# Kernel tuning notes

Hardware: AMD Instinct MI355X
Metric: run time of the kernel (lower is better)

## Reference

```python
import jax, jax.numpy as jnp
import numpy as np

B, S, D, H = 4, 2048, 1024, 16
HD = D // H  # head_dim = 64

def setup_inputs() -> dict:
    key = jax.random.key(0)
    ks = jax.random.split(key, 5)
    scale = 1.0 / np.sqrt(D)
    return {
        "x": jax.random.normal(ks[0], (B, S, D), dtype=jnp.float32),
        "Wqkv": jax.random.normal(ks[1], (D, 3 * D), dtype=jnp.float32) * scale,
        "bqkv": jax.random.normal(ks[2], (3 * D,), dtype=jnp.float32) * 0.01,
        "Wo": jax.random.normal(ks[3], (D, D), dtype=jnp.float32) * scale,
        "bo": jax.random.normal(ks[4], (D,), dtype=jnp.float32) * 0.01,
    }

def reference(x, Wqkv, bqkv, Wo, bo):
    b, s, d = x.shape
    # fused QKV projection: [B,S,3D]
    qkv = jnp.einsum("bsd,de->bse", x, Wqkv) + bqkv
    # [B,S,H,3*HD] -> [B,H,S,3*HD], then chunk into q,k,v per head
    qkv = qkv.reshape(b, s, H, 3 * HD).transpose(0, 2, 1, 3)
    q, k, v = jnp.split(qkv, 3, axis=-1)  # each [B,H,S,HD]
    inv_sqrt_dk = jnp.asarray(1.0 / np.sqrt(HD), dtype=x.dtype)
    scores = jnp.einsum("bhqd,bhkd->bhqk", q, k) * inv_sqrt_dk
    attn = jax.nn.softmax(scores, axis=-1)
    values = jnp.einsum("bhqk,bhkd->bhqd", attn, v)  # [B,H,S,HD]
    # NOTE: source reshapes [B,H,S,HD] -> [B,S,H*HD] WITHOUT permuting back
    # (a quirk of the original code); replicated faithfully.
    values = values.reshape(b, s, d)
    out = jnp.einsum("bsd,de->bse", values, Wo) + bo
    return out
```

## Files before the change

### kernel.cpp

```cpp
#include <hip/hip_runtime.h>
#include <hip/hip_bf16.h>
#include <cstdint>

static constexpr int Bq  = 4;
static constexpr int Sq  = 2048;
static constexpr int Dq  = 1024;
static constexpr int Hq  = 16;
static constexpr int HDq = 64;
static constexpr int ROWS = Bq * Sq;
static constexpr int QKV_N = 3 * Dq;

typedef __bf16 bf16x8 __attribute__((ext_vector_type(8)));
typedef __bf16 bf16x4 __attribute__((ext_vector_type(4)));
typedef float  floatx4 __attribute__((ext_vector_type(4)));

#define MFMA16(a, b, c) __builtin_amdgcn_mfma_f32_16x16x32_bf16((a), (b), (c), 0, 0, 0)

#define QSCALE 0.18033688011112042f

__device__ __forceinline__ void async16(const void* g, void* l) {
    __builtin_amdgcn_global_load_lds(
        (const __attribute__((address_space(1))) uint32_t*)g,
        (__attribute__((address_space(3))) uint32_t*)l, 16, 0, 0);
}

__global__ __launch_bounds__(256) void cvt4_kernel(const float4* __restrict__ in,
                                                   bf16x4* __restrict__ out, int n4) {
    int i = blockIdx.x * 256 + threadIdx.x;
    if (i < n4) {
        float4 v = in[i];
        bf16x4 o;
        o[0] = (__bf16)v.x; o[1] = (__bf16)v.y; o[2] = (__bf16)v.z; o[3] = (__bf16)v.w;
        out[i] = o;
    }
}

__global__ __launch_bounds__(256) void tcvt_kernel(const float* __restrict__ in,
                                                   __bf16* __restrict__ out, int K, int N) {
    __shared__ float t[32][33];
    int n0 = blockIdx.x * 32, k0 = blockIdx.y * 32;
    int c = threadIdx.x & 31, r0 = threadIdx.x >> 5;
#pragma unroll
    for (int rr = 0; rr < 32; rr += 8)
        t[r0 + rr][c] = in[(size_t)(k0 + r0 + rr) * N + n0 + c];
    __syncthreads();
#pragma unroll
    for (int rr = 0; rr < 32; rr += 8)
        out[(size_t)(n0 + r0 + rr) * K + k0 + c] = (__bf16)t[c][r0 + rr];
}

template <int MODE>
__global__ __launch_bounds__(256) void gemm_bt_kernel(const __bf16* __restrict__ A,
                                                      const __bf16* __restrict__ BT,
                                                      const float* __restrict__ bias,
                                                      void* __restrict__ Cout,
                                                      __bf16* __restrict__ Vt,
                                                      int M, int N, int K) {
    __shared__ __bf16 As[128 * 32];
    __shared__ __bf16 Bs[128 * 32];

    const int t = threadIdx.x;
    const int lane = t & 63;
    const int wave = t >> 6;
    const int wm = wave & 1, wn = wave >> 1;
    const int l15 = lane & 15;
    const int kg = (lane >> 4) * 8;

    const int m0 = blockIdx.y * 128;
    const int n0 = blockIdx.x * 128;

    const int srow = t >> 2;
    const int scol = (t & 3) * 8;
    const __bf16* ag = A  + (size_t)(m0 + srow) * K + scol;
    const __bf16* bg = BT + (size_t)(n0 + srow) * K + scol;
    __bf16* al = As + t * 8;
    __bf16* bl = Bs + t * 8;

    floatx4 acc[4][4] = {};

    for (int k0 = 0; k0 < K; k0 += 32) {
        __syncthreads();
        async16(ag + k0,                    al);
        async16(ag + (size_t)64 * K + k0,   al + 2048);
        async16(bg + k0,                    bl);
        async16(bg + (size_t)64 * K + k0,   bl + 2048);
        __syncthreads();

        bf16x8 af[4], bfr[4];
#pragma unroll
        for (int mi = 0; mi < 4; ++mi)
            af[mi] = *(const bf16x8*)(As + (wm * 64 + mi * 16 + l15) * 32 + kg);
#pragma unroll
        for (int ni = 0; ni < 4; ++ni)
            bfr[ni] = *(const bf16x8*)(Bs + (wn * 64 + ni * 16 + l15) * 32 + kg);
#pragma unroll
        for (int mi = 0; mi < 4; ++mi)
#pragma unroll
            for (int ni = 0; ni < 4; ++ni)
                acc[mi][ni] = MFMA16(af[mi], bfr[ni], acc[mi][ni]);
    }

    const int r0 = (lane >> 4) * 4;
    const int wn0 = n0 + wn * 64;

    if (MODE == 2 && (wn0 % 192) == 128) {
#pragma unroll
        for (int ni = 0; ni < 4; ++ni) {
            int col = wn0 + ni * 16 + l15;
            float bv = bias[col];
            int h = col / 192;
            int d = col - h * 192 - 128;
#pragma unroll
            for (int mi = 0; mi < 4; ++mi) {
                int row = m0 + wm * 64 + mi * 16 + r0;
                int b = row >> 11, s = row & 2047;
                bf16x4 vv;
#pragma unroll
                for (int i = 0; i < 4; ++i) vv[i] = (__bf16)(acc[mi][ni][i] + bv);
                *(bf16x4*)(Vt + ((size_t)(b * Hq + h) * HDq + d) * Sq + s) = vv;
            }
        }
    } else {
        const float sc = (MODE == 2 && (wn0 % 192) == 0) ? QSCALE : 1.0f;
#pragma unroll
        for (int ni = 0; ni < 4; ++ni) {
            int col = wn0 + ni * 16 + l15;
            float bv = bias[col];
#pragma unroll
            for (int mi = 0; mi < 4; ++mi) {
#pragma unroll
                for (int i = 0; i < 4; ++i) {
                    int row = m0 + wm * 64 + mi * 16 + r0 + i;
                    float v = (acc[mi][ni][i] + bv) * sc;
                    size_t off = (size_t)row * N + col;
                    if (MODE == 1) ((float*)Cout)[off] = v;
                    else           ((__bf16*)Cout)[off] = (__bf16)v;
                }
            }
        }
    }
}

__global__ __launch_bounds__(256, 4) void attn_kernel(const __bf16* __restrict__ qkv,
                                                      const __bf16* __restrict__ Vt,
                                                      __bf16* __restrict__ v2) {
    const int bh = blockIdx.y;
    const int b = bh >> 4, h = bh & 15;
    const int q0 = blockIdx.x * 128;
    const int tid = threadIdx.x;
    const int lane = tid & 63;
    const int wave = tid >> 6;
    const int l15 = lane & 15;
    const int quad = lane >> 4;
    const int kg = quad * 8;
    const size_t rs = QKV_N;
    const __bf16* base  = qkv + (size_t)b * Sq * rs + (size_t)h * (3 * HDq);
    const __bf16* vbase = Vt + (size_t)bh * HDq * Sq;

    __shared__ alignas(16) __bf16 Ks[64][72];
    __shared__ alignas(16) __bf16 Vs[64][72];
    __shared__ alignas(16) __bf16 PT[8][16][72];

    bf16x8 qa[2][2];
#pragma unroll
    for (int qt = 0; qt < 2; ++qt) {
        const __bf16* qr = base + (size_t)(q0 + qt * 64 + wave * 16 + l15) * rs;
        qa[qt][0] = *(const bf16x8*)(qr + kg);
        qa[qt][1] = *(const bf16x8*)(qr + 32 + kg);
    }

    const int sd = tid >> 2;
    const int sc = (tid & 3) * 8;
    const __bf16* kgp = base + 64 + sc;
    const __bf16* vgp = vbase + (size_t)sd * Sq + sc;

    bf16x8 kr0 = *(const bf16x8*)(kgp + (size_t)sd * rs);
    bf16x8 kr1 = *(const bf16x8*)(kgp + (size_t)sd * rs + 32);
    bf16x8 vr0 = *(const bf16x8*)(vgp);
    bf16x8 vr1 = *(const bf16x8*)(vgp + 32);

    floatx4 o[2][4] = {};
    float l_acc[2] = {0.f, 0.f};

    for (int kt = 0; kt < Sq; kt += 64) {
        __syncthreads();
        *(bf16x8*)(&Ks[sd][sc])      = kr0;
        *(bf16x8*)(&Ks[sd][sc + 32]) = kr1;
        *(bf16x8*)(&Vs[sd][sc])      = vr0;
        *(bf16x8*)(&Vs[sd][sc + 32]) = vr1;
        __syncthreads();

        const int ktn = (kt + 64) & (Sq - 1);
        kr0 = *(const bf16x8*)(kgp + (size_t)(ktn + sd) * rs);
        kr1 = *(const bf16x8*)(kgp + (size_t)(ktn + sd) * rs + 32);
        vr0 = *(const bf16x8*)(vgp + ktn);
        vr1 = *(const bf16x8*)(vgp + ktn + 32);

        floatx4 s[2][4];
#pragma unroll
        for (int tt = 0; tt < 4; ++tt) {
            bf16x8 k0 = *(const bf16x8*)(&Ks[tt * 16 + l15][kg]);
            bf16x8 k1 = *(const bf16x8*)(&Ks[tt * 16 + l15][32 + kg]);
#pragma unroll
            for (int qt = 0; qt < 2; ++qt) {
                floatx4 z = {};
                z = MFMA16(k0, qa[qt][0], z);
                s[qt][tt] = MFMA16(k1, qa[qt][1], z);
            }
        }

#pragma unroll
        for (int qt = 0; qt < 2; ++qt) {
            float lsum = 0.f;
#pragma unroll
            for (int tt = 0; tt < 4; ++tt) {
                bf16x4 pp;
#pragma unroll
                for (int i = 0; i < 4; ++i) {
                    float p = __builtin_amdgcn_exp2f(s[qt][tt][i]);
                    lsum += p;
                    pp[i] = (__bf16)p;
                }
                *(bf16x4*)(&PT[qt * 4 + wave][l15][tt * 16 + quad * 4]) = pp;
            }
            l_acc[qt] += lsum;
        }

#pragma unroll
        for (int ks = 0; ks < 2; ++ks) {
            bf16x8 vb[4];
#pragma unroll
            for (int tt = 0; tt < 4; ++tt)
                vb[tt] = *(const bf16x8*)(&Vs[tt * 16 + l15][ks * 32 + kg]);
#pragma unroll
            for (int qt = 0; qt < 2; ++qt) {
                bf16x8 pa = *(const bf16x8*)(&PT[qt * 4 + wave][l15][ks * 32 + kg]);
#pragma unroll
                for (int tt = 0; tt < 4; ++tt)
                    o[qt][tt] = MFMA16(vb[tt], pa, o[qt][tt]);
            }
        }
    }

    float rinv[2];
#pragma unroll
    for (int qt = 0; qt < 2; ++qt) {
        float l = l_acc[qt];
        l += __shfl_xor(l, 16);
        l += __shfl_xor(l, 32);
        rinv[qt] = 1.0f / l;
    }

#pragma unroll
    for (int qt = 0; qt < 2; ++qt) {
        int q = q0 + qt * 64 + wave * 16 + l15;
        size_t row = (size_t)b * Sq + h * 128 + (q >> 4);
        __bf16* vrow = v2 + row * Dq + (size_t)(q & 15) * 64;
#pragma unroll
        for (int tt = 0; tt < 4; ++tt) {
            bf16x4 ov;
#pragma unroll
            for (int i = 0; i < 4; ++i)
                ov[i] = (__bf16)(o[qt][tt][i] * rinv[qt]);
            *(bf16x4*)(vrow + tt * 16 + quad * 4) = ov;
        }
    }
}

extern "C" void kernel_launch(void* const* d_in, const int* in_sizes, int n_in,
                              void* d_out, int out_size, void* d_ws, size_t ws_size,
                              hipStream_t stream) {
    const float* x    = (const float*)d_in[0];
    const float* Wqkv = (const float*)d_in[1];
    const float* bqkv = (const float*)d_in[2];
    const float* Wo   = (const float*)d_in[3];
    const float* bo   = (const float*)d_in[4];
    float* out = (float*)d_out;

    __bf16* xb    = (__bf16*)d_ws;
    __bf16* WqkvT = xb    + (size_t)ROWS * Dq;
    __bf16* WoT   = WqkvT + (size_t)QKV_N * Dq;
    __bf16* qkvb  = WoT   + (size_t)Dq * Dq;
    __bf16* Vt    = qkvb  + (size_t)ROWS * QKV_N;
    __bf16* v2    = xb;

    const int nx4 = ROWS * Dq / 4;
    cvt4_kernel<<<(nx4 + 255) / 256, 256, 0, stream>>>((const float4*)x, (bf16x4*)xb, nx4);
    tcvt_kernel<<<dim3(QKV_N / 32, Dq / 32), 256, 0, stream>>>(Wqkv, WqkvT, Dq, QKV_N);
    tcvt_kernel<<<dim3(Dq / 32, Dq / 32), 256, 0, stream>>>(Wo, WoT, Dq, Dq);

    gemm_bt_kernel<2><<<dim3(QKV_N / 128, ROWS / 128), 256, 0, stream>>>(
        xb, WqkvT, bqkv, (void*)qkvb, Vt, ROWS, QKV_N, Dq);

    attn_kernel<<<dim3(Sq / 128, Bq * Hq), 256, 0, stream>>>(qkvb, Vt, v2);

    gemm_bt_kernel<1><<<dim3(Dq / 128, ROWS / 128), 256, 0, stream>>>(
        v2, WoT, bo, (void*)out, nullptr, ROWS, Dq, Dq);
}
```

Before: 288.7 us.

## Load K/V fragments directly from global into registers, drop LDS staging and barriers

The attention kernel now has each wave load its K and V MFMA operand fragments straight from global memory into registers, instead of staging K/V tiles through shared memory with two block barriers per key tile. The Vt buffer row pitch is padded to 2112 elements, apparently to avoid cache or channel conflicts across head-dim rows. This removes LDS traffic and synchronisation, but each of the four waves now re-reads the same K/V data from L2/L1 with less coalesced, strided access. The software prefetch of the next tile is also gone, so load latency is exposed unless occupancy hides it. The Vt allocation must match the padded size, which the visible code does not show.

After: 450.8 us. 56.1% more time.

```diff
diff --git a/kernel.cpp b/kernel.cpp
--- a/kernel.cpp
+++ b/kernel.cpp
@@ -9,6 +9,7 @@
 static constexpr int HDq = 64;
 static constexpr int ROWS = Bq * Sq;
 static constexpr int QKV_N = 3 * Dq;
+static constexpr int VP   = 2112;
 
 typedef __bf16 bf16x8 __attribute__((ext_vector_type(8)));
 typedef __bf16 bf16x4 __attribute__((ext_vector_type(4)));
@@ -117,7 +118,7 @@
                 bf16x4 vv;
 #pragma unroll
                 for (int i = 0; i < 4; ++i) vv[i] = (__bf16)(acc[mi][ni][i] + bv);
-                *(bf16x4*)(Vt + ((size_t)(b * Hq + h) * HDq + d) * Sq + s) = vv;
+                *(bf16x4*)(Vt + ((size_t)(b * Hq + h) * HDq + d) * VP + s) = vv;
             }
         }
     } else {
@@ -147,19 +148,16 @@
     const int bh = blockIdx.y;
     const int b = bh >> 4, h = bh & 15;
     const int q0 = blockIdx.x * 128;
-    const int tid = threadIdx.x;
-    const int lane = tid & 63;
-    const int wave = tid >> 6;
+    const int lane = threadIdx.x & 63;
+    const int wave = threadIdx.x >> 6;
     const int l15 = lane & 15;
     const int quad = lane >> 4;
     const int kg = quad * 8;
     const size_t rs = QKV_N;
     const __bf16* base  = qkv + (size_t)b * Sq * rs + (size_t)h * (3 * HDq);
-    const __bf16* vbase = Vt + (size_t)bh * HDq * Sq;
-
-    __shared__ alignas(16) __bf16 Ks[64][72];
-    __shared__ alignas(16) __bf16 Vs[64][72];
-    __shared__ alignas(16) __bf16 PT[8][16][72];
+    const __bf16* vbase = Vt + (size_t)bh * HDq * VP;
+
+    __shared__ alignas(16) __bf16 PT[4][2][16][72];
 
     bf16x8 qa[2][2];
 #pragma unroll
@@ -169,43 +167,41 @@
         qa[qt][1] = *(const bf16x8*)(qr + 32 + kg);
     }
 
-    const int sd = tid >> 2;
-    const int sc = (tid & 3) * 8;
-    const __bf16* kgp = base + 64 + sc;
-    const __bf16* vgp = vbase + (size_t)sd * Sq + sc;
-
-    bf16x8 kr0 = *(const bf16x8*)(kgp + (size_t)sd * rs);
-    bf16x8 kr1 = *(const bf16x8*)(kgp + (size_t)sd * rs + 32);
-    bf16x8 vr0 = *(const bf16x8*)(vgp);
-    bf16x8 vr1 = *(const bf16x8*)(vgp + 32);
+    const __bf16* kp[4];
+    const __bf16* vp[4];
+#pragma unroll
+    for (int tt = 0; tt < 4; ++tt) {
+        kp[tt] = base + HDq + (size_t)(tt * 16 + l15) * rs + kg;
+        vp[tt] = vbase + (size_t)(tt * 16 + l15) * VP + kg;
+    }
 
     floatx4 o[2][4] = {};
     float l_acc[2] = {0.f, 0.f};
 
     for (int kt = 0; kt < Sq; kt += 64) {
-        __syncthreads();
-        *(bf16x8*)(&Ks[sd][sc])      = kr0;
-        *(bf16x8*)(&Ks[sd][sc + 32]) = kr1;
-        *(bf16x8*)(&Vs[sd][sc])      = vr0;
-        *(bf16x8*)(&Vs[sd][sc + 32]) = vr1;
-        __syncthreads();
-
-        const int ktn = (kt + 64) & (Sq - 1);
-        kr0 = *(const bf16x8*)(kgp + (size_t)(ktn + sd) * rs);
-        kr1 = *(const bf16x8*)(kgp + (size_t)(ktn + sd) * rs + 32);
-        vr0 = *(const bf16x8*)(vgp + ktn);
-        vr1 = *(const bf16x8*)(vgp + ktn + 32);
+        bf16x8 ka0[4], ka1[4];
+#pragma unroll
+        for (int tt = 0; tt < 4; ++tt) {
+            ka0[tt] = *(const bf16x8*)(kp[tt]);
+            ka1[tt] = *(const bf16x8*)(kp[tt] + 32);
+            kp[tt] += (size_t)64 * rs;
+        }
+        bf16x8 va0[4], va1[4];
+#pragma unroll
+        for (int tt = 0; tt < 4; ++tt) {
+            va0[tt] = *(const bf16x8*)(vp[tt]);
+            va1[tt] = *(const bf16x8*)(vp[tt] + 32);
+            vp[tt] += 64;
+        }
 
         floatx4 s[2][4];
 #pragma unroll
         for (int tt = 0; tt < 4; ++tt) {
-            bf16x8 k0 = *(const bf16x8*)(&Ks[tt * 16 + l15][kg]);
-            bf16x8 k1 = *(const bf16x8*)(&Ks[tt * 16 + l15][32 + kg]);
 #pragma unroll
             for (int qt = 0; qt < 2; ++qt) {
                 floatx4 z = {};
-                z = MFMA16(k0, qa[qt][0], z);
-                s[qt][tt] = MFMA16(k1, qa[qt][1], z);
+                z = MFMA16(ka0[tt], qa[qt][0], z);
+                s[qt][tt] = MFMA16(ka1[tt], qa[qt][1], z);
             }
         }
 
@@ -221,23 +217,19 @@
                     lsum += p;
                     pp[i] = (__bf16)p;
                 }
-                *(bf16x4*)(&PT[qt * 4 + wave][l15][tt * 16 + quad * 4]) = pp;
+                *(bf16x4*)(&PT[wave][qt][l15][tt * 16 + quad * 4]) = pp;
             }
             l_acc[qt] += lsum;
         }
 
 #pragma unroll
-        for (int ks = 0; ks < 2; ++ks) {
-            bf16x8 vb[4];
-#pragma unroll
-            for (int tt = 0; tt < 4; ++tt)
-                vb[tt] = *(const bf16x8*)(&Vs[tt * 16 + l15][ks * 32 + kg]);
-#pragma unroll
-            for (int qt = 0; qt < 2; ++qt) {
-                bf16x8 pa = *(const bf16x8*)(&PT[qt * 4 + wave][l15][ks * 32 + kg]);
-#pragma unroll
-                for (int tt = 0; tt < 4; ++tt)
-                    o[qt][tt] = MFMA16(vb[tt], pa, o[qt][tt]);
+        for (int qt = 0; qt < 2; ++qt) {
+            bf16x8 pa0 = *(const bf16x8*)(&PT[wave][qt][l15][kg]);
+            bf16x8 pa1 = *(const bf16x8*)(&PT[wave][qt][l15][32 + kg]);
+#pragma unroll
+            for (int tt = 0; tt < 4; ++tt) {
+                o[qt][tt] = MFMA16(va0[tt], pa0, o[qt][tt]);
+                o[qt][tt] = MFMA16(va1[tt], pa1, o[qt][tt]);
             }
         }
     }
```

## Enlarge attention query tile, double-buffer K/V in LDS, pad V transpose pitch

Applied to the files above, without the earlier changes.

Each attention block now handles 256 queries (4 query tiles per wave), so every K/V tile loaded into LDS is reused across twice as many queries. K/V shared buffers are double-buffered so only one barrier per iteration is needed. The transposed V buffer uses a padded row pitch to reduce memory channel conflicts. This trades higher register use, lower occupancy and fewer blocks per CU for more reuse and fewer syncs. It also slightly enlarges the workspace needed.

Result: slower. 313.4 us (+8.6%).

```diff
diff --git a/kernel.cpp b/kernel.cpp
--- a/kernel.cpp
+++ b/kernel.cpp
@@ -9,6 +9,7 @@
 static constexpr int HDq = 64;
 static constexpr int ROWS = Bq * Sq;
 static constexpr int QKV_N = 3 * Dq;
+static constexpr int VP   = 2112;
 
 typedef __bf16 bf16x8 __attribute__((ext_vector_type(8)));
 typedef __bf16 bf16x4 __attribute__((ext_vector_type(4)));
@@ -117,7 +118,7 @@
                 bf16x4 vv;
 #pragma unroll
                 for (int i = 0; i < 4; ++i) vv[i] = (__bf16)(acc[mi][ni][i] + bv);
-                *(bf16x4*)(Vt + ((size_t)(b * Hq + h) * HDq + d) * Sq + s) = vv;
+                *(bf16x4*)(Vt + ((size_t)(b * Hq + h) * HDq + d) * VP + s) = vv;
             }
         }
     } else {
@@ -141,12 +142,12 @@
     }
 }
 
-__global__ __launch_bounds__(256, 4) void attn_kernel(const __bf16* __restrict__ qkv,
-                                                      const __bf16* __restrict__ Vt,
-                                                      __bf16* __restrict__ v2) {
+__global__ __launch_bounds__(256) void attn_kernel(const __bf16* __restrict__ qkv,
+                                                   const __bf16* __restrict__ Vt,
+                                                   __bf16* __restrict__ v2) {
     const int bh = blockIdx.y;
     const int b = bh >> 4, h = bh & 15;
-    const int q0 = blockIdx.x * 128;
+    const int q0 = blockIdx.x * 256;
     const int tid = threadIdx.x;
     const int lane = tid & 63;
     const int wave = tid >> 6;
@@ -155,15 +156,15 @@
     const int kg = quad * 8;
     const size_t rs = QKV_N;
     const __bf16* base  = qkv + (size_t)b * Sq * rs + (size_t)h * (3 * HDq);
-    const __bf16* vbase = Vt + (size_t)bh * HDq * Sq;
-
-    __shared__ alignas(16) __bf16 Ks[64][72];
-    __shared__ alignas(16) __bf16 Vs[64][72];
-    __shared__ alignas(16) __bf16 PT[8][16][72];
-
-    bf16x8 qa[2][2];
-#pragma unroll
-    for (int qt = 0; qt < 2; ++qt) {
+    const __bf16* vbase = Vt + (size_t)bh * HDq * VP;
+
+    __shared__ alignas(16) __bf16 Ks[2][64][72];
+    __shared__ alignas(16) __bf16 Vs[2][64][72];
+    __shared__ alignas(16) __bf16 PT[4][4][16][72];
+
+    bf16x8 qa[4][2];
+#pragma unroll
+    for (int qt = 0; qt < 4; ++qt) {
         const __bf16* qr = base + (size_t)(q0 + qt * 64 + wave * 16 + l15) * rs;
         qa[qt][0] = *(const bf16x8*)(qr + kg);
         qa[qt][1] = *(const bf16x8*)(qr + 32 + kg);
@@ -171,80 +172,81 @@
 
     const int sd = tid >> 2;
     const int sc = (tid & 3) * 8;
-    const __bf16* kgp = base + 64 + sc;
-    const __bf16* vgp = vbase + (size_t)sd * Sq + sc;
-
-    bf16x8 kr0 = *(const bf16x8*)(kgp + (size_t)sd * rs);
-    bf16x8 kr1 = *(const bf16x8*)(kgp + (size_t)sd * rs + 32);
+    const __bf16* kgp = base + 64 + (size_t)sd * rs + sc;
+    const __bf16* vgp = vbase + (size_t)sd * VP + sc;
+
+    bf16x8 kr0 = *(const bf16x8*)(kgp);
+    bf16x8 kr1 = *(const bf16x8*)(kgp + 32);
     bf16x8 vr0 = *(const bf16x8*)(vgp);
     bf16x8 vr1 = *(const bf16x8*)(vgp + 32);
 
-    floatx4 o[2][4] = {};
-    float l_acc[2] = {0.f, 0.f};
+    floatx4 o[4][4] = {};
+    float l_acc[4] = {};
 
     for (int kt = 0; kt < Sq; kt += 64) {
+        const int buf = (kt >> 6) & 1;
+        *(bf16x8*)(&Ks[buf][sd][sc])      = kr0;
+        *(bf16x8*)(&Ks[buf][sd][sc + 32]) = kr1;
+        *(bf16x8*)(&Vs[buf][sd][sc])      = vr0;
+        *(bf16x8*)(&Vs[buf][sd][sc + 32]) = vr1;
         __syncthreads();
-        *(bf16x8*)(&Ks[sd][sc])      = kr0;
-        *(bf16x8*)(&Ks[sd][sc + 32]) = kr1;
-        *(bf16x8*)(&Vs[sd][sc])      = vr0;
-        *(bf16x8*)(&Vs[sd][sc + 32]) = vr1;
-        __syncthreads();
 
         const int ktn = (kt + 64) & (Sq - 1);
-        kr0 = *(const bf16x8*)(kgp + (size_t)(ktn + sd) * rs);
-        kr1 = *(const bf16x8*)(kgp + (size_t)(ktn + sd) * rs + 32);
+        kr0 = *(const bf16x8*)(kgp + (size_t)ktn * rs);
+        kr1 = *(const bf16x8*)(kgp + (size_t)ktn * rs + 32);
         vr0 = *(const bf16x8*)(vgp + ktn);
         vr1 = *(const bf16x8*)(vgp + ktn + 32);
 
-        floatx4 s[2][4];
+        bf16x8 ka0[4], ka1[4];
 #pragma unroll
         for (int tt = 0; tt < 4; ++tt) {
-            bf16x8 k0 = *(const bf16x8*)(&Ks[tt * 16 + l15][kg]);
-            bf16x8 k1 = *(const bf16x8*)(&Ks[tt * 16 + l15][32 + kg]);
-#pragma unroll
-            for (int qt = 0; qt < 2; ++qt) {
+            ka0[tt] = *(const bf16x8*)(&Ks[buf][tt * 16 + l15][kg]);
+            ka1[tt] = *(const bf16x8*)(&Ks[buf][tt * 16 + l15][32 + kg]);
+        }
+
+#pragma unroll
+        for (int qt = 0; qt < 4; ++qt) {
+            floatx4 s[4];
+#pragma unroll
+            for (int tt = 0; tt < 4; ++tt) {
                 floatx4 z = {};
-                z = MFMA16(k0, qa[qt][0], z);
-                s[qt][tt] = MFMA16(k1, qa[qt][1], z);
-            }
-        }
-
-#pragma unroll
-        for (int qt = 0; qt < 2; ++qt) {
+                z = MFMA16(ka0[tt], qa[qt][0], z);
+                s[tt] = MFMA16(ka1[tt], qa[qt][1], z);
+            }
             float lsum = 0.f;
 #pragma unroll
             for (int tt = 0; tt < 4; ++tt) {
                 bf16x4 pp;
 #pragma unroll
                 for (int i = 0; i < 4; ++i) {
-                    float p = __builtin_amdgcn_exp2f(s[qt][tt][i]);
+                    float p = __builtin_amdgcn_exp2f(s[tt][i]);
                     lsum += p;
                     pp[i] = (__bf16)p;
                 }
-                *(bf16x4*)(&PT[qt * 4 + wave][l15][tt * 16 + quad * 4]) = pp;
+                *(bf16x4*)(&PT[wave][qt][l15][tt * 16 + quad * 4]) = pp;
             }
             l_acc[qt] += lsum;
         }
 
 #pragma unroll
         for (int ks = 0; ks < 2; ++ks) {
-            bf16x8 vb[4];
+            bf16x8 va[4];
 #pragma unroll
             for (int tt = 0; tt < 4; ++tt)
-                vb[tt] = *(const bf16x8*)(&Vs[tt * 16 + l15][ks * 32 + kg]);
-#pragma unroll
-            for (int qt = 0; qt < 2; ++qt) {
-                bf16x8 pa = *(const bf16x8*)(&PT[qt * 4 + wave][l15][ks * 32 + kg]);
+                va[tt] = *(const bf16x8*)(&Vs[buf][tt * 16 + l15][ks * 32 + kg]);
+#pragma unroll
+            for (int qt = 0; qt < 4; ++qt) {
+                bf16x8 pa = *(const bf16x8*)(&PT[wave][qt][l15][ks * 32 + kg]);
 #pragma unroll
                 for (int tt = 0; tt < 4; ++tt)
-                    o[qt][tt] = MFMA16(vb[tt], pa, o[qt][tt]);
-            }
-        }
-    }
-
-    float rinv[2];
-#pragma unroll
-    for (int qt = 0; qt < 2; ++qt) {
+                    o[qt][tt] = MFMA16(va[tt], pa, o[qt][tt]);
+            }
+        }
+    }
+
+    float rinv[4];
+#pragma unroll
+    for (int qt = 0; qt < 4; ++qt) {
         float l = l_acc[qt];
         l += __shfl_xor(l, 16);
         l += __shfl_xor(l, 32);
@@ -252,7 +254,7 @@
     }
 
 #pragma unroll
-    for (int qt = 0; qt < 2; ++qt) {
+    for (int qt = 0; qt < 4; ++qt) {
         int q = q0 + qt * 64 + wave * 16 + l15;
         size_t row = (size_t)b * Sq + h * 128 + (q >> 4);
         __bf16* vrow = v2 + row * Dq + (size_t)(q & 15) * 64;
@@ -292,7 +294,7 @@
     gemm_bt_kernel<2><<<dim3(QKV_N / 128, ROWS / 128), 256, 0, stream>>>(
         xb, WqkvT, bqkv, (void*)qkvb, Vt, ROWS, QKV_N, Dq);
 
-    attn_kernel<<<dim3(Sq / 128, Bq * Hq), 256, 0, stream>>>(qkvb, Vt, v2);
+    attn_kernel<<<dim3(Sq / 256, Bq * Hq), 256, 0, stream>>>(qkvb, Vt, v2);
 
     gemm_bt_kernel<1><<<dim3(Dq / 128, ROWS / 128), 256, 0, stream>>>(
         v2, WoT, bo, (void*)out, nullptr, ROWS, Dq, Dq);
```
